# Kernel optimization log

Hardware: AMD Instinct MI355X
Metric: run time of the kernel (lower is better)

The kernel has to match this reference:

```python
import jax, jax.numpy as jnp
import numpy as np

INPUT, HIDDEN = 8, 16

def setup_inputs() -> dict:
    key = jax.random.key(0)
    ks = jax.random.split(key, 7)
    s_ih = 1.0 / np.sqrt(HIDDEN)
    x = jax.random.normal(ks[0], (8192, 512, INPUT), dtype=jnp.float32)
    W_ih = jax.random.uniform(ks[1], (HIDDEN, INPUT), jnp.float32, -s_ih, s_ih)
    W_hh = jax.random.uniform(ks[2], (HIDDEN, HIDDEN), jnp.float32, -s_ih, s_ih)
    b_ih = jax.random.uniform(ks[3], (HIDDEN,), jnp.float32, -s_ih, s_ih)
    b_hh = jax.random.uniform(ks[4], (HIDDEN,), jnp.float32, -s_ih, s_ih)
    s_fc = 1.0 / np.sqrt(HIDDEN)
    fc_w = jax.random.uniform(ks[5], (1, HIDDEN), jnp.float32, -s_fc, s_fc)
    fc_b = jax.random.uniform(ks[6], (1,), jnp.float32, -s_fc, s_fc)
    return {"x": x, "W_ih": W_ih, "W_hh": W_hh, "b_ih": b_ih, "b_hh": b_hh, "fc_w": fc_w, "fc_b": fc_b}

def reference(x, W_ih, W_hh, b_ih, b_hh, fc_w, fc_b):
    B, T, _ = x.shape
    # Precompute input projection for all timesteps: [B, T, H]
    xp = jnp.einsum('bti,hi->bth', x, W_ih) + b_ih + b_hh
    h0 = jnp.zeros((B, HIDDEN), dtype=x.dtype)

    def step(h, xt):
        h_new = jnp.tanh(xt + h @ W_hh.T)
        return h_new, None

    h_last, _ = jax.lax.scan(step, h0, jnp.swapaxes(xp, 0, 1))
    return h_last @ fc_w.T + fc_b  # [B, 1]
```

## Files before the change

kernel.cpp:

```cpp
#include <hip/hip_runtime.h>
#include <stdint.h>


#define RNN_B   8192
#define RNN_T   512
#define RNN_IN  8
#define RNN_H   16
#define TC      32
#define NB      16
#define XSTRIDE 264
#define NTILE   (RNN_T / TC)
#define BUFSZ   (NB * XSTRIDE)

#if defined(__has_builtin)
#if __has_builtin(__builtin_amdgcn_mov_dpp)
#define ROR16(x, N) ((uint32_t)__builtin_amdgcn_mov_dpp((int)(x), 0x120 + (N), 0xF, 0xF, false))
#endif
#endif
#ifndef ROR16
#define ROR16(x, N) ((uint32_t)__builtin_amdgcn_update_dpp(0, (int)(x), 0x120 + (N), 0xF, 0xF, false))
#endif

__device__ __forceinline__ void gather16(uint32_t in, uint32_t v[16]) {
    v[0]  = in;
    v[8]  = ROR16(v[0], 8);
    v[4]  = ROR16(v[0], 4);
    v[12] = ROR16(v[8], 4);
    v[2]  = ROR16(v[0], 2);
    v[6]  = ROR16(v[4], 2);
    v[10] = ROR16(v[8], 2);
    v[14] = ROR16(v[12], 2);
    v[1]  = ROR16(v[0], 1);
    v[3]  = ROR16(v[2], 1);
    v[5]  = ROR16(v[4], 1);
    v[7]  = ROR16(v[6], 1);
    v[9]  = ROR16(v[8], 1);
    v[11] = ROR16(v[10], 1);
    v[13] = ROR16(v[12], 1);
    v[15] = ROR16(v[14], 1);
}

__device__ __forceinline__ void stage_tile(const float* __restrict__ x,
                                           float* lds_base, int b0, int t0,
                                           int wv, int lane)
{
#pragma unroll
    for (int p = 0; p < 4; ++p) {
        const int row = wv + 4 * p;
        const float* gp = x + ((size_t)(b0 + row) * RNN_T + t0) * RNN_IN + lane * 4;
        float* lp = lds_base + row * XSTRIDE;
        __builtin_amdgcn_global_load_lds(
            (const __attribute__((address_space(1))) uint32_t*)gp,
            (__attribute__((address_space(3))) uint32_t*)lp,
            16, 0, 0);
    }
}

__global__ __launch_bounds__(256, 2) void rnn_fused_kernel(
    const float* __restrict__ x,
    const float* __restrict__ W_ih,
    const float* __restrict__ W_hh,
    const float* __restrict__ b_ih,
    const float* __restrict__ b_hh,
    const float* __restrict__ fc_w,
    const float* __restrict__ fc_b,
    float* __restrict__ out)
{
    __shared__ float xs[2 * BUFSZ];

    const int tid  = (int)threadIdx.x;
    const int j    = tid & 15;
    const int g    = tid >> 4;
    const int wv   = tid >> 6;
    const int lane = tid & 63;
    const int b0   = (int)blockIdx.x * NB;
    const int b    = b0 + g;

    uint32_t sv[16];
    gather16((uint32_t)j, sv);
    float whh[RNN_H];
#pragma unroll
    for (int m = 0; m < 16; ++m) whh[m] = W_hh[j * RNN_H + (int)sv[m]];

    float wih[RNN_IN];
#pragma unroll
    for (int i = 0; i < RNN_IN; i += 4) {
        float4 w = *(const float4*)(W_ih + j * RNN_IN + i);
        wih[i] = w.x; wih[i+1] = w.y; wih[i+2] = w.z; wih[i+3] = w.w;
    }
    const float bias = b_ih[j] + b_hh[j];

    stage_tile(x, xs, b0, 0, wv, lane);
    __syncthreads();

    float hn = 0.0f;

    for (int tile = 0; tile < NTILE; ++tile) {
        const int cur = tile & 1;
        if (tile + 1 < NTILE)
            stage_tile(x, xs + (cur ^ 1) * BUFSZ, b0, (tile + 1) * TC, wv, lane);

        const float* xg = xs + cur * BUFSZ + g * XSTRIDE;

#pragma unroll 8
        for (int tt = 0; tt < TC; ++tt) {
            const float* xp = xg + tt * RNN_IN;
            const float4 xa = *(const float4*)(xp);
            const float4 xb = *(const float4*)(xp + 4);

            uint32_t v[16];
            gather16(__float_as_uint(hn), v);

            float a0 = fmaf(wih[0], xa.x, bias);
            a0 = fmaf(wih[1], xa.y, a0);
            a0 = fmaf(wih[2], xa.z, a0);
            a0 = fmaf(wih[3], xa.w, a0);
            a0 = fmaf(whh[0], __uint_as_float(v[0]), a0);
            a0 = fmaf(whh[1], __uint_as_float(v[1]), a0);
            a0 = fmaf(whh[2], __uint_as_float(v[2]), a0);
            a0 = fmaf(whh[3], __uint_as_float(v[3]), a0);

            float a1 = wih[4] * xb.x;
            a1 = fmaf(wih[5], xb.y, a1);
            a1 = fmaf(wih[6], xb.z, a1);
            a1 = fmaf(wih[7], xb.w, a1);
            a1 = fmaf(whh[4], __uint_as_float(v[4]), a1);
            a1 = fmaf(whh[5], __uint_as_float(v[5]), a1);
            a1 = fmaf(whh[6], __uint_as_float(v[6]), a1);
            a1 = fmaf(whh[7], __uint_as_float(v[7]), a1);

            float a2 = whh[8] * __uint_as_float(v[8]);
            a2 = fmaf(whh[9],  __uint_as_float(v[9]),  a2);
            a2 = fmaf(whh[10], __uint_as_float(v[10]), a2);
            a2 = fmaf(whh[11], __uint_as_float(v[11]), a2);

            float a3 = whh[12] * __uint_as_float(v[12]);
            a3 = fmaf(whh[13], __uint_as_float(v[13]), a3);
            a3 = fmaf(whh[14], __uint_as_float(v[14]), a3);
            a3 = fmaf(whh[15], __uint_as_float(v[15]), a3);

            const float s = (a0 + a2) + (a1 + a3);

            const float e  = __builtin_amdgcn_exp2f(s * 2.8853900817779268f);
            const float r  = __builtin_amdgcn_rcpf(e + 1.0f);
            hn = fmaf(-2.0f, r, 1.0f);
        }
        __syncthreads();
    }

    float vsum = hn * fc_w[j];
    vsum += __shfl_xor(vsum, 1);
    vsum += __shfl_xor(vsum, 2);
    vsum += __shfl_xor(vsum, 4);
    vsum += __shfl_xor(vsum, 8);
    if (j == 0) out[b] = vsum + fc_b[0];
}

extern "C" void kernel_launch(void* const* d_in, const int* in_sizes, int n_in,
                              void* d_out, int out_size, void* d_ws, size_t ws_size,
                              hipStream_t stream)
{
    const float* x    = (const float*)d_in[0];
    const float* W_ih = (const float*)d_in[1];
    const float* W_hh = (const float*)d_in[2];
    const float* b_ih = (const float*)d_in[3];
    const float* b_hh = (const float*)d_in[4];
    const float* fc_w = (const float*)d_in[5];
    const float* fc_b = (const float*)d_in[6];
    float* out = (float*)d_out;

    dim3 grid(RNN_B / NB);
    dim3 block(256);
    rnn_fused_kernel<<<grid, block, 0, stream>>>(x, W_ih, W_hh, b_ih, b_hh, fc_w, fc_b, out);
}
```

Measured before the change: 250.3 us.

## Split each hidden-unit dot product across two 16-lane halves with permlane swap

Each batch element now uses 32 lanes instead of 16. Each half computes half of the recurrent and input dot product and the two partial sums are combined with a permlane16 swap. This halves the DPP gather chain and the FMA count per lane on the serial critical path. The tanh scaling constants are folded into the weights and bias, and the state is carried as the sigmoid-like value so one FMA per step disappears. Blocks now cover 8 batch elements, doubling the grid size, and the launch bounds target 4 blocks per SIMD instead of 2, which raises register pressure and thread count in exchange for shorter per-step latency.

```diff
diff --git a/kernel.cpp b/kernel.cpp
--- a/kernel.cpp
+++ b/kernel.cpp
@@ -7,10 +7,12 @@
 #define RNN_IN  8
 #define RNN_H   16
 #define TC      32
-#define NB      16
+#define NE      8
 #define XSTRIDE 264
 #define NTILE   (RNN_T / TC)
-#define BUFSZ   (NB * XSTRIDE)
+#define BUFSZ   (NE * XSTRIDE)
+
+typedef uint32_t u32x2 __attribute__((ext_vector_type(2)));
 
 #if defined(__has_builtin)
 #if __has_builtin(__builtin_amdgcn_mov_dpp)
@@ -21,23 +23,25 @@
 #define ROR16(x, N) ((uint32_t)__builtin_amdgcn_update_dpp(0, (int)(x), 0x120 + (N), 0xF, 0xF, false))
 #endif
 
-__device__ __forceinline__ void gather16(uint32_t in, uint32_t v[16]) {
-    v[0]  = in;
-    v[8]  = ROR16(v[0], 8);
-    v[4]  = ROR16(v[0], 4);
-    v[12] = ROR16(v[8], 4);
-    v[2]  = ROR16(v[0], 2);
-    v[6]  = ROR16(v[4], 2);
-    v[10] = ROR16(v[8], 2);
-    v[14] = ROR16(v[12], 2);
-    v[1]  = ROR16(v[0], 1);
-    v[3]  = ROR16(v[2], 1);
-    v[5]  = ROR16(v[4], 1);
-    v[7]  = ROR16(v[6], 1);
-    v[9]  = ROR16(v[8], 1);
-    v[11] = ROR16(v[10], 1);
-    v[13] = ROR16(v[12], 1);
-    v[15] = ROR16(v[14], 1);
+__device__ __forceinline__ void half_gather(uint32_t vb, uint32_t u[8]) {
+    u[0] = vb;
+    u[4] = ROR16(vb, 4);
+    u[2] = ROR16(vb, 2);
+    u[6] = ROR16(u[4], 2);
+    u[1] = ROR16(vb, 1);
+    u[3] = ROR16(u[2], 1);
+    u[5] = ROR16(u[4], 1);
+    u[7] = ROR16(u[6], 1);
+}
+
+__device__ __forceinline__ float pair_sum(float s) {
+#if defined(__has_builtin) && __has_builtin(__builtin_amdgcn_permlane16_swap)
+    u32x2 pr = __builtin_amdgcn_permlane16_swap(__float_as_uint(s), __float_as_uint(s),
+                                                false, false);
+    return __uint_as_float(pr.x) + __uint_as_float(pr.y);
+#else
+    return s + __uint_as_float((uint32_t)__shfl_xor((int)__float_as_uint(s), 16));
+#endif
 }
 
 __device__ __forceinline__ void stage_tile(const float* __restrict__ x,
@@ -45,8 +49,8 @@
                                            int wv, int lane)
 {
 #pragma unroll
-    for (int p = 0; p < 4; ++p) {
-        const int row = wv + 4 * p;
+    for (int p = 0; p < 2; ++p) {
+        const int row = 2 * wv + p;
         const float* gp = x + ((size_t)(b0 + row) * RNN_T + t0) * RNN_IN + lane * 4;
         float* lp = lds_base + row * XSTRIDE;
         __builtin_amdgcn_global_load_lds(
@@ -56,7 +60,7 @@
     }
 }
 
-__global__ __launch_bounds__(256, 2) void rnn_fused_kernel(
+__global__ __launch_bounds__(256, 4) void rnn_fused_kernel(
     const float* __restrict__ x,
     const float* __restrict__ W_ih,
     const float* __restrict__ W_hh,
@@ -70,90 +74,92 @@
 
     const int tid  = (int)threadIdx.x;
     const int j    = tid & 15;
-    const int g    = tid >> 4;
+    const int r    = (tid >> 4) & 1;
+    const int g    = tid >> 5;
     const int wv   = tid >> 6;
     const int lane = tid & 63;
-    const int b0   = (int)blockIdx.x * NB;
-    const int b    = b0 + g;
+    const int b0   = (int)blockIdx.x * NE;
+    const bool rsel = (r == 1);
 
-    uint32_t sv[16];
-    gather16((uint32_t)j, sv);
-    float whh[RNN_H];
+    const float C = 2.8853900817779268f;
+
+    uint32_t sv[8];
+    {
+        uint32_t t8 = ROR16((uint32_t)j, 8);
+        uint32_t vb = rsel ? t8 : (uint32_t)j;
+        half_gather(vb, sv);
+    }
+
+    float whh_l[8];
+    float rsum = 0.0f;
 #pragma unroll
-    for (int m = 0; m < 16; ++m) whh[m] = W_hh[j * RNN_H + (int)sv[m]];
+    for (int i = 0; i < 8; ++i) {
+        float w = W_hh[j * RNN_H + (int)sv[i]];
+        whh_l[i] = -2.0f * C * w;
+        rsum += w;
+    }
+    float bias_l = C * rsum;
+    if (!rsel) bias_l += C * (b_ih[j] + b_hh[j]);
 
-    float wih[RNN_IN];
-#pragma unroll
-    for (int i = 0; i < RNN_IN; i += 4) {
-        float4 w = *(const float4*)(W_ih + j * RNN_IN + i);
-        wih[i] = w.x; wih[i+1] = w.y; wih[i+2] = w.z; wih[i+3] = w.w;
+    float wih_l[4];
+    {
+        float4 w = *(const float4*)(W_ih + j * RNN_IN + 4 * r);
+        wih_l[0] = C * w.x; wih_l[1] = C * w.y; wih_l[2] = C * w.z; wih_l[3] = C * w.w;
     }
-    const float bias = b_ih[j] + b_hh[j];
 
     stage_tile(x, xs, b0, 0, wv, lane);
     __syncthreads();
 
-    float hn = 0.0f;
+    float rv = 0.5f;
 
     for (int tile = 0; tile < NTILE; ++tile) {
         const int cur = tile & 1;
         if (tile + 1 < NTILE)
             stage_tile(x, xs + (cur ^ 1) * BUFSZ, b0, (tile + 1) * TC, wv, lane);
 
-        const float* xg = xs + cur * BUFSZ + g * XSTRIDE;
+        const float* xg = xs + cur * BUFSZ + g * XSTRIDE + 4 * r;
 
 #pragma unroll 8
         for (int tt = 0; tt < TC; ++tt) {
-            const float* xp = xg + tt * RNN_IN;
-            const float4 xa = *(const float4*)(xp);
-            const float4 xb = *(const float4*)(xp + 4);
+            const float4 xv = *(const float4*)(xg + tt * RNN_IN);
 
-            uint32_t v[16];
-            gather16(__float_as_uint(hn), v);
+            const uint32_t rb = __float_as_uint(rv);
+            const uint32_t t8 = ROR16(rb, 8);
+            const uint32_t vb = rsel ? t8 : rb;
+            uint32_t u[8];
+            half_gather(vb, u);
 
-            float a0 = fmaf(wih[0], xa.x, bias);
-            a0 = fmaf(wih[1], xa.y, a0);
-            a0 = fmaf(wih[2], xa.z, a0);
-            a0 = fmaf(wih[3], xa.w, a0);
-            a0 = fmaf(whh[0], __uint_as_float(v[0]), a0);
-            a0 = fmaf(whh[1], __uint_as_float(v[1]), a0);
-            a0 = fmaf(whh[2], __uint_as_float(v[2]), a0);
-            a0 = fmaf(whh[3], __uint_as_float(v[3]), a0);
+            float c0 = fmaf(wih_l[0], xv.x, bias_l);
+            c0 = fmaf(wih_l[1], xv.y, c0);
+            c0 = fmaf(wih_l[2], xv.z, c0);
+            c0 = fmaf(wih_l[3], xv.w, c0);
 
-            float a1 = wih[4] * xb.x;
-            a1 = fmaf(wih[5], xb.y, a1);
-            a1 = fmaf(wih[6], xb.z, a1);
-            a1 = fmaf(wih[7], xb.w, a1);
-            a1 = fmaf(whh[4], __uint_as_float(v[4]), a1);
-            a1 = fmaf(whh[5], __uint_as_float(v[5]), a1);
-            a1 = fmaf(whh[6], __uint_as_float(v[6]), a1);
-            a1 = fmaf(whh[7], __uint_as_float(v[7]), a1);
+            float c1 = whh_l[0] * __uint_as_float(u[0]);
+            c1 = fmaf(whh_l[1], __uint_as_float(u[1]), c1);
+            c1 = fmaf(whh_l[2], __uint_as_float(u[2]), c1);
+            c1 = fmaf(whh_l[3], __uint_as_float(u[3]), c1);
 
-            float a2 = whh[8] * __uint_as_float(v[8]);
-            a2 = fmaf(whh[9],  __uint_as_float(v[9]),  a2);
-            a2 = fmaf(whh[10], __uint_as_float(v[10]), a2);
-            a2 = fmaf(whh[11], __uint_as_float(v[11]), a2);
+            float c2 = whh_l[4] * __uint_as_float(u[4]);
+            c2 = fmaf(whh_l[5], __uint_as_float(u[5]), c2);
+            c2 = fmaf(whh_l[6], __uint_as_float(u[6]), c2);
+            c2 = fmaf(whh_l[7], __uint_as_float(u[7]), c2);
 
-            float a3 = whh[12] * __uint_as_float(v[12]);
-            a3 = fmaf(whh[13], __uint_as_float(v[13]), a3);
-            a3 = fmaf(whh[14], __uint_as_float(v[14]), a3);
-            a3 = fmaf(whh[15], __uint_as_float(v[15]), a3);
+            const float sp   = (c0 + c1) + c2;
+            const float stot = pair_sum(sp);
 
-            const float s = (a0 + a2) + (a1 + a3);
-
-            const float e  = __builtin_amdgcn_exp2f(s * 2.8853900817779268f);
-            const float r  = __builtin_amdgcn_rcpf(e + 1.0f);
-            hn = fmaf(-2.0f, r, 1.0f);
+            const float e = __builtin_amdgcn_exp2f(stot);
+            rv = __builtin_amdgcn_rcpf(e + 1.0f);
         }
         __syncthreads();
     }
 
-    float vsum = hn * fc_w[j];
+    const float h = fmaf(-2.0f, rv, 1.0f);
+    float vsum = h * fc_w[j];
     vsum += __shfl_xor(vsum, 1);
     vsum += __shfl_xor(vsum, 2);
     vsum += __shfl_xor(vsum, 4);
     vsum += __shfl_xor(vsum, 8);
-    if (j == 0) out[b] = vsum + fc_b[0];
+    if ((tid & 31) == 0) out[b0 + g] = vsum + fc_b[0];
 }
 
 extern "C" void kernel_launch(void* const* d_in, const int* in_sizes, int n_in,
@@ -169,7 +175,7 @@
     const float* fc_b = (const float*)d_in[6];
     float* out = (float*)d_out;
 
-    dim3 grid(RNN_B / NB);
+    dim3 grid(RNN_B / NE);
     dim3 block(256);
     rnn_fused_kernel<<<grid, block, 0, stream>>>(x, W_ih, W_hh, b_ih, b_hh, fc_w, fc_b, out);
 }
```

Result: slower. 278.6 us (+11.3%).

## Fold tanh affine into weights, precompute input projection per tile, use 64-thread blocks

Applied to the files above, without the earlier changes.

Rewrites the recurrence to carry r = 1/(1+exp(2s)) instead of h, folding the -2 scale, the +1 offset and the exp2 constant into W_hh, W_ih and the bias. This removes a multiply and an FMA from the serial dependency chain of each step. The input projection for a whole 32-step tile is computed up front into registers, off the critical path, before the next tile is prefetched. Blocks shrink to one 64-thread wave handling 4 batch rows, which gives independent per-wave scheduling without cross-wave barriers but uses more registers per thread and more blocks.

```diff
diff --git a/kernel.cpp b/kernel.cpp
--- a/kernel.cpp
+++ b/kernel.cpp
@@ -7,10 +7,10 @@
 #define RNN_IN  8
 #define RNN_H   16
 #define TC      32
-#define NB      16
-#define XSTRIDE 264
+#define NE      4
+#define XROW    260
 #define NTILE   (RNN_T / TC)
-#define BUFSZ   (NB * XSTRIDE)
+#define BUFSZ   (NE * XROW)
 
 #if defined(__has_builtin)
 #if __has_builtin(__builtin_amdgcn_mov_dpp)
@@ -40,15 +40,14 @@
     v[15] = ROR16(v[14], 1);
 }
 
-__device__ __forceinline__ void stage_tile(const float* __restrict__ x,
-                                           float* lds_base, int b0, int t0,
-                                           int wv, int lane)
+static __device__ __forceinline__ void stage(const float* __restrict__ x,
+                                             float* lds_base, int b0, int t0,
+                                             int lane)
 {
 #pragma unroll
-    for (int p = 0; p < 4; ++p) {
-        const int row = wv + 4 * p;
-        const float* gp = x + ((size_t)(b0 + row) * RNN_T + t0) * RNN_IN + lane * 4;
-        float* lp = lds_base + row * XSTRIDE;
+    for (int e = 0; e < NE; ++e) {
+        const float* gp = x + ((size_t)(b0 + e) * RNN_T + t0) * RNN_IN + lane * 4;
+        float* lp = lds_base + e * XROW;
         __builtin_amdgcn_global_load_lds(
             (const __attribute__((address_space(1))) uint32_t*)gp,
             (__attribute__((address_space(3))) uint32_t*)lp,
@@ -56,7 +55,7 @@
     }
 }
 
-__global__ __launch_bounds__(256, 2) void rnn_fused_kernel(
+__global__ __launch_bounds__(64) void rnn_valu_kernel(
     const float* __restrict__ x,
     const float* __restrict__ W_ih,
     const float* __restrict__ W_hh,
@@ -66,94 +65,102 @@
     const float* __restrict__ fc_b,
     float* __restrict__ out)
 {
-    __shared__ float xs[2 * BUFSZ];
+    __shared__ __align__(16) float xs[2 * BUFSZ];
 
-    const int tid  = (int)threadIdx.x;
-    const int j    = tid & 15;
-    const int g    = tid >> 4;
-    const int wv   = tid >> 6;
-    const int lane = tid & 63;
-    const int b0   = (int)blockIdx.x * NB;
-    const int b    = b0 + g;
+    const int lane = (int)threadIdx.x;
+    const int j    = lane & 15;
+    const int g    = lane >> 4;
+    const int b0   = (int)blockIdx.x * NE;
+    const float C2 = 2.8853900817779268f;
 
     uint32_t sv[16];
     gather16((uint32_t)j, sv);
+
     float whh[RNN_H];
+    float rsum = 0.0f;
 #pragma unroll
-    for (int m = 0; m < 16; ++m) whh[m] = W_hh[j * RNN_H + (int)sv[m]];
+    for (int m = 0; m < 16; ++m) {
+        const float w = W_hh[j * RNN_H + (int)sv[m]];
+        whh[m] = -2.0f * C2 * w;
+        rsum  += w;
+    }
+    const float bias_l = C2 * (b_ih[j] + b_hh[j]) + C2 * rsum;
 
     float wih[RNN_IN];
 #pragma unroll
     for (int i = 0; i < RNN_IN; i += 4) {
-        float4 w = *(const float4*)(W_ih + j * RNN_IN + i);
-        wih[i] = w.x; wih[i+1] = w.y; wih[i+2] = w.z; wih[i+3] = w.w;
+        const float4 w = *(const float4*)(W_ih + j * RNN_IN + i);
+        wih[i] = C2 * w.x; wih[i+1] = C2 * w.y; wih[i+2] = C2 * w.z; wih[i+3] = C2 * w.w;
     }
-    const float bias = b_ih[j] + b_hh[j];
 
-    stage_tile(x, xs, b0, 0, wv, lane);
+    stage(x, xs, b0, 0, lane);
     __syncthreads();
 
-    float hn = 0.0f;
+    float rv = 0.5f;
 
     for (int tile = 0; tile < NTILE; ++tile) {
         const int cur = tile & 1;
+
+        const float* xg = xs + cur * BUFSZ + g * XROW;
+        float xp[TC];
+#pragma unroll
+        for (int tt = 0; tt < TC; ++tt) {
+            const float4 xa = *(const float4*)(xg + tt * 8);
+            const float4 xb = *(const float4*)(xg + tt * 8 + 4);
+            float t0 = fmaf(wih[0], xa.x, bias_l);
+            t0 = fmaf(wih[1], xa.y, t0);
+            t0 = fmaf(wih[2], xa.z, t0);
+            t0 = fmaf(wih[3], xa.w, t0);
+            float t1 = wih[4] * xb.x;
+            t1 = fmaf(wih[5], xb.y, t1);
+            t1 = fmaf(wih[6], xb.z, t1);
+            t1 = fmaf(wih[7], xb.w, t1);
+            xp[tt] = t0 + t1;
+        }
+
         if (tile + 1 < NTILE)
-            stage_tile(x, xs + (cur ^ 1) * BUFSZ, b0, (tile + 1) * TC, wv, lane);
+            stage(x, xs + (cur ^ 1) * BUFSZ, b0, (tile + 1) * TC, lane);
 
-        const float* xg = xs + cur * BUFSZ + g * XSTRIDE;
+#pragma unroll
+        for (int tt = 0; tt < TC; ++tt) {
+            uint32_t v[16];
+            gather16(__float_as_uint(rv), v);
 
-#pragma unroll 8
-        for (int tt = 0; tt < TC; ++tt) {
-            const float* xp = xg + tt * RNN_IN;
-            const float4 xa = *(const float4*)(xp);
-            const float4 xb = *(const float4*)(xp + 4);
+            float c0 = fmaf(whh[0],  __uint_as_float(v[0]),  xp[tt]);
+            c0 = fmaf(whh[8],  __uint_as_float(v[8]),  c0);
+            c0 = fmaf(whh[4],  __uint_as_float(v[4]),  c0);
+            c0 = fmaf(whh[2],  __uint_as_float(v[2]),  c0);
 
-            uint32_t v[16];
-            gather16(__float_as_uint(hn), v);
+            float c1 = whh[12] * __uint_as_float(v[12]);
+            c1 = fmaf(whh[6],  __uint_as_float(v[6]),  c1);
+            c1 = fmaf(whh[10], __uint_as_float(v[10]), c1);
+            c1 = fmaf(whh[14], __uint_as_float(v[14]), c1);
 
-            float a0 = fmaf(wih[0], xa.x, bias);
-            a0 = fmaf(wih[1], xa.y, a0);
-            a0 = fmaf(wih[2], xa.z, a0);
-            a0 = fmaf(wih[3], xa.w, a0);
-            a0 = fmaf(whh[0], __uint_as_float(v[0]), a0);
-            a0 = fmaf(whh[1], __uint_as_float(v[1]), a0);
-            a0 = fmaf(whh[2], __uint_as_float(v[2]), a0);
-            a0 = fmaf(whh[3], __uint_as_float(v[3]), a0);
+            float c2 = whh[1] * __uint_as_float(v[1]);
+            c2 = fmaf(whh[3],  __uint_as_float(v[3]),  c2);
+            c2 = fmaf(whh[5],  __uint_as_float(v[5]),  c2);
+            c2 = fmaf(whh[7],  __uint_as_float(v[7]),  c2);
 
-            float a1 = wih[4] * xb.x;
-            a1 = fmaf(wih[5], xb.y, a1);
-            a1 = fmaf(wih[6], xb.z, a1);
-            a1 = fmaf(wih[7], xb.w, a1);
-            a1 = fmaf(whh[4], __uint_as_float(v[4]), a1);
-            a1 = fmaf(whh[5], __uint_as_float(v[5]), a1);
-            a1 = fmaf(whh[6], __uint_as_float(v[6]), a1);
-            a1 = fmaf(whh[7], __uint_as_float(v[7]), a1);
+            float c3 = whh[9] * __uint_as_float(v[9]);
+            c3 = fmaf(whh[11], __uint_as_float(v[11]), c3);
+            c3 = fmaf(whh[13], __uint_as_float(v[13]), c3);
+            c3 = fmaf(whh[15], __uint_as_float(v[15]), c3);
 
-            float a2 = whh[8] * __uint_as_float(v[8]);
-            a2 = fmaf(whh[9],  __uint_as_float(v[9]),  a2);
-            a2 = fmaf(whh[10], __uint_as_float(v[10]), a2);
-            a2 = fmaf(whh[11], __uint_as_float(v[11]), a2);
+            const float s = (c0 + c1) + (c2 + c3);
 
-            float a3 = whh[12] * __uint_as_float(v[12]);
-            a3 = fmaf(whh[13], __uint_as_float(v[13]), a3);
-            a3 = fmaf(whh[14], __uint_as_float(v[14]), a3);
-            a3 = fmaf(whh[15], __uint_as_float(v[15]), a3);
-
-            const float s = (a0 + a2) + (a1 + a3);
-
-            const float e  = __builtin_amdgcn_exp2f(s * 2.8853900817779268f);
-            const float r  = __builtin_amdgcn_rcpf(e + 1.0f);
-            hn = fmaf(-2.0f, r, 1.0f);
+            const float e = __builtin_amdgcn_exp2f(s);
+            rv = __builtin_amdgcn_rcpf(e + 1.0f);
         }
         __syncthreads();
     }
 
-    float vsum = hn * fc_w[j];
+    const float h = fmaf(-2.0f, rv, 1.0f);
+    float vsum = h * fc_w[j];
     vsum += __shfl_xor(vsum, 1);
     vsum += __shfl_xor(vsum, 2);
     vsum += __shfl_xor(vsum, 4);
     vsum += __shfl_xor(vsum, 8);
-    if (j == 0) out[b] = vsum + fc_b[0];
+    if (j == 0) out[b0 + g] = vsum + fc_b[0];
 }
 
 extern "C" void kernel_launch(void* const* d_in, const int* in_sizes, int n_in,
@@ -169,7 +176,7 @@
     const float* fc_b = (const float*)d_in[6];
     float* out = (float*)d_out;
 
-    dim3 grid(RNN_B / NB);
-    dim3 block(256);
-    rnn_fused_kernel<<<grid, block, 0, stream>>>(x, W_ih, W_hh, b_ih, b_hh, fc_w, fc_b, out);
+    dim3 grid(RNN_B / NE);
+    dim3 block(64);
+    rnn_valu_kernel<<<grid, block, 0, stream>>>(x, W_ih, W_hh, b_ih, b_hh, fc_w, fc_b, out);
 }
```

Measured after the change: 256.8 us. +2.6%, slower.
